# Kernel tuning notes

Hardware: AMD Instinct MI355X
Metric: run time of the kernel (lower is better)

## Reference

```python
import jax, jax.numpy as jnp
import numpy as np

N_NODES = 50000
N_EDGES = 800000
EMB = 128
HID = [128, 128]
OUT = 64
CE = 8  # stand-in for CROSS_ENTROPY_INDEXES: first 8 output columns get sigmoid


def _linear_params(key, d_in, d_out):
    k1, k2 = jax.random.split(key)
    s = 1.0 / np.sqrt(d_in)
    w = jax.random.uniform(k1, (d_in, d_out), minval=-s, maxval=s, dtype=jnp.float32)
    b = jax.random.uniform(k2, (d_out,), minval=-s, maxval=s, dtype=jnp.float32)
    return w, b


def setup_inputs() -> dict:
    key = jax.random.key(0)
    ks = jax.random.split(key, 16)
    z = jax.random.normal(ks[0], (N_NODES, EMB), dtype=jnp.float32)
    edge_index = jax.random.randint(ks[1], (2, N_EDGES), 0, N_NODES, dtype=jnp.int64)
    # SAGEConv params: neighbor weight (with bias) + root weight
    w1_n, b1 = _linear_params(ks[2], EMB, HID[0])
    w1_r, _ = _linear_params(ks[3], EMB, HID[0])
    w2_n, b2 = _linear_params(ks[4], HID[0], HID[1])
    w2_r, _ = _linear_params(ks[5], HID[0], HID[1])
    wf_n, bf = _linear_params(ks[6], HID[1], OUT)
    wf_r, _ = _linear_params(ks[7], HID[1], OUT)
    # initial residual linears: emb -> hid[1], emb -> out
    w_res1, b_res1 = _linear_params(ks[8], EMB, HID[1])
    w_res2, b_res2 = _linear_params(ks[9], EMB, OUT)
    return dict(z=z, edge_index=edge_index,
                w1_n=w1_n, w1_r=w1_r, b1=b1,
                w2_n=w2_n, w2_r=w2_r, b2=b2,
                wf_n=wf_n, wf_r=wf_r, bf=bf,
                w_res1=w_res1, b_res1=b_res1,
                w_res2=w_res2, b_res2=b_res2)


def _sage(x, src, dst, w_n, w_r, b, n_nodes):
    # mean-aggregate neighbor features at target nodes, then affine combine with root
    msg = x[src]                                        # [E, d]
    agg = jax.ops.segment_sum(msg, dst, num_segments=n_nodes)
    deg = jax.ops.segment_sum(jnp.ones_like(dst, dtype=x.dtype), dst, num_segments=n_nodes)
    mean = agg / jnp.maximum(deg, 1.0)[:, None]
    return mean @ w_n + x @ w_r + b


def reference(z, edge_index, w1_n, w1_r, b1, w2_n, w2_r, b2, wf_n, wf_r, bf,
              w_res1, b_res1, w_res2, b_res2):
    n = z.shape[0]
    src, dst = edge_index[0], edge_index[1]
    h = jax.nn.relu(_sage(z, src, dst, w1_n, w1_r, b1, n))
    # mid layer (dropout is identity in eval) + initial residual
    h = jax.nn.relu(_sage(h, src, dst, w2_n, w2_r, b2, n))
    h = h + (z @ w_res1 + b_res1)
    # final conv + final residual
    h = _sage(h, src, dst, wf_n, wf_r, bf, n)
    h = h + (z @ w_res2 + b_res2)
    # sigmoid on cross-entropy columns
    h = h.at[:, :CE].set(jax.nn.sigmoid(h[:, :CE]))
    return h
```

## Files before the change

kernel.cpp:

```cpp
#include <hip/hip_runtime.h>
#include <hip/hip_bf16.h>
#include <math.h>

#define NN 50000
#define NE 800000
#define NB 391
#define EPB 6250

typedef short bf16x8 __attribute__((ext_vector_type(8)));
typedef float f32x4 __attribute__((ext_vector_type(4)));
typedef unsigned short us4 __attribute__((ext_vector_type(4)));
typedef unsigned short us8 __attribute__((ext_vector_type(8)));
typedef unsigned int u32x4 __attribute__((ext_vector_type(4)));

__device__ __forceinline__ float bf2f(unsigned short u) {
  union { unsigned int i; float f; } x; x.i = ((unsigned int)u) << 16; return x.f;
}
__device__ __forceinline__ unsigned short f2bf(float f) {
  union { float f; unsigned int i; } x; x.f = f;
  unsigned int i = x.i;
  unsigned int r = i + 0x7FFF + ((i >> 16) & 1);
  return (unsigned short)(r >> 16);
}
__device__ __forceinline__ unsigned long long pk64(f32x4 v) {
  union { us4 s; unsigned long long u; } x;
  x.s[0] = f2bf(v[0]); x.s[1] = f2bf(v[1]); x.s[2] = f2bf(v[2]); x.s[3] = f2bf(v[3]);
  return x.u;
}
__device__ __forceinline__ us4 pack4(f32x4 v) {
  us4 o; o[0] = f2bf(v[0]); o[1] = f2bf(v[1]); o[2] = f2bf(v[2]); o[3] = f2bf(v[3]);
  return o;
}

__global__ __launch_bounds__(512) void bscan_kernel(const int* __restrict__ bhist,
                                                    int* __restrict__ bucket_off,
                                                    int* __restrict__ gcur) {
  __shared__ int s[512];
  int t = threadIdx.x;
  int v = (t < NB) ? bhist[t] : 0;
  s[t] = v; __syncthreads();
  for (int off = 1; off < 512; off <<= 1) {
    int x = (t >= off) ? s[t - off] : 0;
    __syncthreads();
    s[t] += x;
    __syncthreads();
  }
  if (t < NB) { bucket_off[t] = s[t] - v; gcur[t] = 0; }
  if (t == NB - 1) bucket_off[NB] = s[t];
}

__global__ __launch_bounds__(256) void bscat_kernel(const int* __restrict__ srcn,
                                                    const int* __restrict__ dstn,
                                                    const int* __restrict__ bucket_off,
                                                    int* __restrict__ gcur,
                                                    unsigned long long* __restrict__ ebuf) {
  __shared__ int hist[NB];
  __shared__ int base[NB];
  for (int i = threadIdx.x; i < NB; i += 256) hist[i] = 0;
  __syncthreads();
  int e0 = blockIdx.x * EPB;
  for (int i = threadIdx.x; i < EPB; i += 256)
    atomicAdd(&hist[dstn[e0 + i] >> 7], 1);
  __syncthreads();
  for (int i = threadIdx.x; i < NB; i += 256) {
    int c = hist[i];
    base[i] = c ? (bucket_off[i] + atomicAdd(&gcur[i], c)) : 0;
  }
  __syncthreads();
  for (int i = threadIdx.x; i < EPB; i += 256) {
    int s = srcn[e0 + i], d = dstn[e0 + i];
    int b = d >> 7;
    int pos = atomicSub(&hist[b], 1) - 1;
    ebuf[(size_t)base[b] + pos] = ((unsigned long long)(unsigned)d << 32) | (unsigned)s;
  }
}

__global__ __launch_bounds__(256) void bfill_kernel(const unsigned long long* __restrict__ ebuf,
                                                    const int* __restrict__ bucket_off,
                                                    int* __restrict__ rowoff,
                                                    int* __restrict__ csr) {
  int b = blockIdx.x;
  int bo = bucket_off[b], cnt = bucket_off[b + 1] - bo;
  __shared__ int ndeg[128], noff[128];
  int t = threadIdx.x;
  if (t < 128) ndeg[t] = 0;
  __syncthreads();
  for (int i = t; i < cnt; i += 256)
    atomicAdd(&ndeg[(int)(ebuf[bo + i] >> 32) & 127], 1);
  __syncthreads();
  if (t < 128) noff[t] = ndeg[t];
  __syncthreads();
  for (int off = 1; off < 128; off <<= 1) {
    int x = 0;
    if (t < 128 && t >= off) x = noff[t - off];
    __syncthreads();
    if (t < 128 && t >= off) noff[t] += x;
    __syncthreads();
  }
  if (t < 128) {
    int ex = noff[t] - ndeg[t];
    noff[t] = ex;
    int node = b * 128 + t;
    if (node < NN) rowoff[node] = bo + ex;
  }
  if (b == NB - 1 && t == 0) rowoff[NN] = NE;
  __syncthreads();
  for (int i = t; i < cnt; i += 256) {
    unsigned long long e = ebuf[bo + i];
    int dl = (int)(e >> 32) & 127;
    int pos = atomicSub(&ndeg[dl], 1) - 1;
    csr[bo + noff[dl] + pos] = (int)(unsigned)e;
  }
}

__global__ __launch_bounds__(256) void setup_kernel(
    const float* __restrict__ z, unsigned short* __restrict__ A1,
    const float* __restrict__ w1n, const float* __restrict__ w1r,
    const float* __restrict__ w2n, const float* __restrict__ w2r,
    const float* __restrict__ wfn, const float* __restrict__ wfr,
    const float* __restrict__ wr1, const float* __restrict__ wr2,
    unsigned short* __restrict__ Bp1, unsigned short* __restrict__ Bp2,
    unsigned short* __restrict__ Bp3,
    const int* __restrict__ dstn, int* __restrict__ bhist) {
  __shared__ int h[NB];
  int b = blockIdx.x;
  if (b < 6250) {
    int i = b * 256 + threadIdx.x;
    if (i >= NN * 128 / 4) return;
    int i4 = i * 4;
    int row = i4 >> 7, c = i4 & 127;
    f32x4 v = *(const f32x4*)(z + i4);
    us4 o = { f2bf(v[0]), f2bf(v[1]), f2bf(v[2]), f2bf(v[3]) };
    *(us4*)(A1 + (size_t)row * 256 + 128 + c) = o;
  } else if (b < 6314) {
    int g = (b - 6250) * 256 + threadIdx.x;
    unsigned short* D; int NT, fi;
    int which;
    if      (g < 10240) { fi = g;         D = Bp1; NT = 20; which = 1; }
    else if (g < 14336) { fi = g - 10240; D = Bp2; NT = 8;  which = 2; }
    else if (g < 16384) { fi = g - 14336; D = Bp3; NT = 4;  which = 3; }
    else return;
    int lane = fi & 63, t = fi >> 6;
    int nt = t % NT, k0i = t / NT;
    int m = lane & 15, q = lane >> 4;
    int kb = k0i * 32 + q * 8;
    int n = nt * 16 + m;
    int hi = (kb >= 128);
    int k0_ = kb - (hi ? 128 : 0);
    const float* W = nullptr; int Nseg = 128; int nn = n;
    if (which == 1) {
      if (n < 128)      { W = hi ? w1r : w1n; nn = n; Nseg = 128; }
      else if (n < 256) { W = hi ? wr1 : nullptr; nn = n - 128; Nseg = 128; }
      else              { W = hi ? wr2 : nullptr; nn = n - 256; Nseg = 64; }
    } else if (which == 2) { W = hi ? w2r : w2n; Nseg = 128; }
    else                   { W = hi ? wfr : wfn; Nseg = 64; }
    unsigned short o[8];
#pragma unroll
    for (int j = 0; j < 8; j++)
      o[j] = W ? f2bf(W[(size_t)(k0_ + j) * Nseg + nn]) : (unsigned short)0;
    *(us8*)(D + (size_t)fi * 8) = *(const us8*)o;
  } else {
    for (int i = threadIdx.x; i < NB; i += 256) h[i] = 0;
    __syncthreads();
    int e0 = (b - 6314) * EPB;
    for (int i = threadIdx.x; i < EPB; i += 256)
      atomicAdd(&h[dstn[e0 + i] >> 7], 1);
    __syncthreads();
    for (int i = threadIdx.x; i < NB; i += 256)
      if (h[i]) atomicAdd(&bhist[i], h[i]);
  }
}

__global__ __launch_bounds__(256) void agg_kernel(const unsigned short* __restrict__ feat, int fstride,
                                                  unsigned short* __restrict__ outm, int ostride,
                                                  const int* __restrict__ rowoff,
                                                  const int* __restrict__ csr) {
  int wave = threadIdx.x >> 6, lane = threadIdx.x & 63;
  int node = blockIdx.x * 4 + wave;
  if (node >= NN) return;
  int beg = rowoff[node], end = rowoff[node + 1];
  int g = lane >> 4;
  int c = (lane & 15) << 3;
  float a[8];
#pragma unroll
  for (int i = 0; i < 8; i++) a[i] = 0.f;
  int e1 = end - 1;
  for (int j = beg + g; j < end; j += 16) {
    int j1 = (j + 4 < e1) ? j + 4 : e1;
    int j2 = (j + 8 < e1) ? j + 8 : e1;
    int j3 = (j + 12 < e1) ? j + 12 : e1;
    int s0 = csr[j], s1 = csr[j1], s2 = csr[j2], s3 = csr[j3];
    float w1 = (j + 4 < end) ? 1.f : 0.f;
    float w2 = (j + 8 < end) ? 1.f : 0.f;
    float w3 = (j + 12 < end) ? 1.f : 0.f;
    u32x4 v0 = *(const u32x4*)(feat + (size_t)s0 * fstride + c);
    u32x4 v1 = *(const u32x4*)(feat + (size_t)s1 * fstride + c);
    u32x4 v2 = *(const u32x4*)(feat + (size_t)s2 * fstride + c);
    u32x4 v3 = *(const u32x4*)(feat + (size_t)s3 * fstride + c);
#pragma unroll
    for (int i = 0; i < 4; i++) {
      float l0 = bf2f((unsigned short)(v0[i] & 0xffff));
      float h0 = bf2f((unsigned short)(v0[i] >> 16));
      l0 = fmaf(w1, bf2f((unsigned short)(v1[i] & 0xffff)), l0);
      h0 = fmaf(w1, bf2f((unsigned short)(v1[i] >> 16)), h0);
      l0 = fmaf(w2, bf2f((unsigned short)(v2[i] & 0xffff)), l0);
      h0 = fmaf(w2, bf2f((unsigned short)(v2[i] >> 16)), h0);
      l0 = fmaf(w3, bf2f((unsigned short)(v3[i] & 0xffff)), l0);
      h0 = fmaf(w3, bf2f((unsigned short)(v3[i] >> 16)), h0);
      a[2*i] += l0;
      a[2*i+1] += h0;
    }
  }
#pragma unroll
  for (int i = 0; i < 8; i++) {
    a[i] += __shfl_xor(a[i], 16, 64);
    a[i] += __shfl_xor(a[i], 32, 64);
  }
  if (g == 0) {
    float inv = 1.f / fmaxf((float)(end - beg), 1.f);
    unsigned int o[4];
#pragma unroll
    for (int i = 0; i < 4; i++)
      o[i] = ((unsigned int)f2bf(a[2*i+1] * inv) << 16) | f2bf(a[2*i] * inv);
    *(u32x4*)(outm + (size_t)node * ostride + c) = *(const u32x4*)o;
  }
}

__global__ __launch_bounds__(256) void gemm1_kernel(
    const unsigned short* __restrict__ A,
    const unsigned short* __restrict__ Bp,
    const float* __restrict__ b1, const float* __restrict__ br1, const float* __restrict__ br2,
    unsigned short* __restrict__ h1out,
    unsigned short* __restrict__ res1, unsigned short* __restrict__ res2)
{
  const int NT = 20, TILES = 4;
  __shared__ unsigned short Bs[TILES * 8 * 512];
  int tid = threadIdx.x;
  int wave = tid >> 6, lane = tid & 63;
  int xg = blockIdx.x;
  int ybase = xg * TILES;
  int row0 = blockIdx.y * 128 + wave * 16;
  int m = lane & 15, q = lane >> 4;
  const float* bias; unsigned short* dst; int dstride, cbb; int relu;
  if (xg < 2)      { bias = b1 + xg * 64;        dst = h1out; dstride = 256; cbb = xg * 64;        relu = 1; }
  else if (xg < 4) { bias = br1 + (xg - 2) * 64; dst = res1;  dstride = 128; cbb = (xg - 2) * 64;  relu = 0; }
  else             { bias = br2;                 dst = res2;  dstride = 64;  cbb = 0;              relu = 0; }

  const unsigned short* arow0 = A + (size_t)(row0 + m) * 256 + q * 8;
  const unsigned short* arow1 = arow0 + 64 * 256;
  bf16x8 af0[8], af1[8];
#pragma unroll
  for (int k0i = 0; k0i < 8; ++k0i) {
    af0[k0i] = *(const bf16x8*)(arow0 + k0i * 32);
    af1[k0i] = *(const bf16x8*)(arow1 + k0i * 32);
  }
#pragma unroll
  for (int i = tid; i < TILES * 64 * 8; i += 256) {
    int k0i = i / (TILES * 64), r = i % (TILES * 64);
    *(us8*)(Bs + (size_t)k0i * TILES * 512 + (size_t)r * 8) =
        *(const us8*)(Bp + ((size_t)k0i * NT + ybase) * 512 + (size_t)r * 8);
  }
  __syncthreads();
  f32x4 acc[2][TILES];
#pragma unroll
  for (int h = 0; h < 2; h++)
#pragma unroll
    for (int i = 0; i < TILES; i++) acc[h][i] = (f32x4){0.f, 0.f, 0.f, 0.f};
#pragma unroll
  for (int k0i = 0; k0i < 8; ++k0i) {
    const unsigned short* bk = Bs + (size_t)k0i * TILES * 512 + lane * 8;
#pragma unroll
    for (int s = 0; s < TILES; ++s) {
      bf16x8 bfr = *(const bf16x8*)(bk + s * 512);
      acc[0][s] = __builtin_amdgcn_mfma_f32_16x16x32_bf16(bfr, af0[k0i], acc[0][s], 0, 0, 0);
      acc[1][s] = __builtin_amdgcn_mfma_f32_16x16x32_bf16(bfr, af1[k0i], acc[1][s], 0, 0, 0);
    }
  }
  int src0 = m + ((q & 1) ? 32 : 0);
#pragma unroll
  for (int h = 0; h < 2; h++) {
    int row = row0 + h * 64 + m;
#pragma unroll
    for (int p = 0; p < 2; p++) {
      f32x4 v0 = acc[h][2 * p], v1 = acc[h][2 * p + 1];
      f32x4 bb0 = *(const f32x4*)(bias + 32 * p + 4 * q);
      f32x4 bb1 = *(const f32x4*)(bias + 32 * p + 16 + 4 * q);
#pragma unroll
      for (int r = 0; r < 4; r++) { v0[r] += bb0[r]; v1[r] += bb1[r]; }
      if (relu) {
#pragma unroll
        for (int r = 0; r < 4; r++) { v0[r] = fmaxf(v0[r], 0.f); v1[r] = fmaxf(v1[r], 0.f); }
      }
      unsigned long long d0 = pk64(v0), d1 = pk64(v1);
      unsigned long long a0 = __shfl(d0, src0, 64);
      unsigned long long b0 = __shfl(d0, src0 + 16, 64);
      unsigned long long a1 = __shfl(d1, src0, 64);
      unsigned long long b1v = __shfl(d1, src0 + 16, 64);
      unsigned long long lo = (q >> 1) ? a1 : a0;
      unsigned long long hi = (q >> 1) ? b1v : b0;
      if (row < NN) {
        unsigned long long ov[2] = { lo, hi };
        *(us8*)(dst + (size_t)row * dstride + cbb + 32 * p + 8 * q) = *(const us8*)ov;
      }
    }
  }
}

__global__ __launch_bounds__(256) void gemm2_kernel(
    const unsigned short* __restrict__ A,
    const unsigned short* __restrict__ Bp,
    const float* __restrict__ b2,
    const unsigned short* __restrict__ res1,
    unsigned short* __restrict__ out_bf)
{
  const int NT = 8, TILES = 4;
  __shared__ unsigned short Bs[TILES * 8 * 512];
  int tid = threadIdx.x;
  int wave = tid >> 6, lane = tid & 63;
  int xg = blockIdx.x;
  int ybase = xg * TILES;
  int cbb = xg * 64;
  const float* bias = b2 + cbb;
  int row0 = blockIdx.y * 128 + wave * 16;
  int m = lane & 15, q = lane >> 4;
  const unsigned short* arow0 = A + (size_t)(row0 + m) * 256 + q * 8;
  const unsigned short* arow1 = arow0 + 64 * 256;
  bf16x8 af0[8], af1[8];
#pragma unroll
  for (int k0i = 0; k0i < 8; ++k0i) {
    af0[k0i] = *(const bf16x8*)(arow0 + k0i * 32);
    af1[k0i] = *(const bf16x8*)(arow1 + k0i * 32);
  }
#pragma unroll
  for (int i = tid; i < TILES * 64 * 8; i += 256) {
    int k0i = i / (TILES * 64), r = i % (TILES * 64);
    *(us8*)(Bs + (size_t)k0i * TILES * 512 + (size_t)r * 8) =
        *(const us8*)(Bp + ((size_t)k0i * NT + ybase) * 512 + (size_t)r * 8);
  }
  __syncthreads();
  f32x4 acc[2][TILES];
#pragma unroll
  for (int h = 0; h < 2; h++)
#pragma unroll
    for (int i = 0; i < TILES; i++) acc[h][i] = (f32x4){0.f, 0.f, 0.f, 0.f};
#pragma unroll
  for (int k0i = 0; k0i < 8; ++k0i) {
    const unsigned short* bk = Bs + (size_t)k0i * TILES * 512 + lane * 8;
#pragma unroll
    for (int s = 0; s < TILES; ++s) {
      bf16x8 bfr = *(const bf16x8*)(bk + s * 512);
      acc[0][s] = __builtin_amdgcn_mfma_f32_16x16x32_bf16(bfr, af0[k0i], acc[0][s], 0, 0, 0);
      acc[1][s] = __builtin_amdgcn_mfma_f32_16x16x32_bf16(bfr, af1[k0i], acc[1][s], 0, 0, 0);
    }
  }
  int src0 = m + ((q & 1) ? 32 : 0);
#pragma unroll
  for (int h = 0; h < 2; h++) {
    int row = row0 + h * 64 + m;
#pragma unroll
    for (int p = 0; p < 2; p++) {
      f32x4 v0 = acc[h][2 * p], v1 = acc[h][2 * p + 1];
      f32x4 bb0 = *(const f32x4*)(bias + 32 * p + 4 * q);
      f32x4 bb1 = *(const f32x4*)(bias + 32 * p + 16 + 4 * q);
#pragma unroll
      for (int r = 0; r < 4; r++) {
        v0[r] = fmaxf(v0[r] + bb0[r], 0.f);
        v1[r] = fmaxf(v1[r] + bb1[r], 0.f);
      }
      unsigned long long d0 = pk64(v0), d1 = pk64(v1);
      unsigned long long a0 = __shfl(d0, src0, 64);
      unsigned long long b0 = __shfl(d0, src0 + 16, 64);
      unsigned long long a1 = __shfl(d1, src0, 64);
      unsigned long long b1v = __shfl(d1, src0 + 16, 64);
      unsigned long long lo = (q >> 1) ? a1 : a0;
      unsigned long long hi = (q >> 1) ? b1v : b0;
      if (row < NN) {
        size_t off = cbb + 32 * p + 8 * q;
        us8 rv = *(const us8*)(res1 + (size_t)row * 128 + off);
        unsigned long long ov[2] = { lo, hi };
        unsigned short* e = (unsigned short*)ov;
#pragma unroll
        for (int r = 0; r < 8; r++) e[r] = f2bf(bf2f(e[r]) + bf2f(rv[r]));
        *(us8*)(out_bf + (size_t)row * 256 + off) = *(const us8*)ov;
      }
    }
  }
}

__global__ __launch_bounds__(256) void gemm3_kernel(
    const unsigned short* __restrict__ A,
    const unsigned short* __restrict__ Bp,
    const float* __restrict__ bias,
    const unsigned short* __restrict__ res2,
    float* __restrict__ out_f)
{
  const int NT = 4, TILES = 4;
  __shared__ unsigned short Bs[TILES * 8 * 512];
  int tid = threadIdx.x;
  int wave = tid >> 6, lane = tid & 63;
  int row0 = blockIdx.y * 64 + wave * 16;
  int m = lane & 15, q = lane >> 4;
  const unsigned short* arow = A + (size_t)(row0 + m) * 256 + q * 8;
  bf16x8 af[8];
#pragma unroll
  for (int k0i = 0; k0i < 8; ++k0i) af[k0i] = *(const bf16x8*)(arow + k0i * 32);
#pragma unroll
  for (int i = tid; i < TILES * 64 * 8; i += 256) {
    int k0i = i / (TILES * 64), r = i % (TILES * 64);
    *(us8*)(Bs + (size_t)k0i * TILES * 512 + (size_t)r * 8) =
        *(const us8*)(Bp + ((size_t)k0i * NT) * 512 + (size_t)r * 8);
  }
  __syncthreads();
  f32x4 acc[TILES];
#pragma unroll
  for (int i = 0; i < TILES; i++) acc[i] = (f32x4){0.f, 0.f, 0.f, 0.f};
#pragma unroll
  for (int k0i = 0; k0i < 8; ++k0i) {
    const unsigned short* bk = Bs + (size_t)k0i * TILES * 512 + lane * 8;
#pragma unroll
    for (int s = 0; s < TILES; ++s) {
      bf16x8 bfr = *(const bf16x8*)(bk + s * 512);
      acc[s] = __builtin_amdgcn_mfma_f32_16x16x32_bf16(bfr, af[k0i], acc[s], 0, 0, 0);
    }
  }
  int row = row0 + m;
  if (row >= NN) return;
  int cb = q * 4;
#pragma unroll
  for (int s = 0; s < TILES; ++s) {
    int col = s * 16 + cb;
    f32x4 v = acc[s];
    f32x4 bb = *(const f32x4*)(bias + col);
    us4 rv = *(const us4*)(res2 + (size_t)row * 64 + col);
#pragma unroll
    for (int r = 0; r < 4; r++) v[r] += bb[r] + bf2f(rv[r]);
    if (col < 8) {
#pragma unroll
      for (int r = 0; r < 4; r++) v[r] = 1.f / (1.f + __expf(-v[r]));
    }
    *(f32x4*)(out_f + (size_t)row * 64 + col) = v;
  }
}

extern "C" void kernel_launch(void* const* d_in, const int* in_sizes, int n_in,
                              void* d_out, int out_size, void* d_ws, size_t ws_size,
                              hipStream_t stream) {
  const float* z   = (const float*)d_in[0];
  const int*   edge = (const int*)d_in[1];
  const int*   srcn = edge;
  const int*   dstn = edge + NE;
  const float* w1n = (const float*)d_in[2];
  const float* w1r = (const float*)d_in[3];
  const float* b1  = (const float*)d_in[4];
  const float* w2n = (const float*)d_in[5];
  const float* w2r = (const float*)d_in[6];
  const float* b2  = (const float*)d_in[7];
  const float* wfn = (const float*)d_in[8];
  const float* wfr = (const float*)d_in[9];
  const float* bfb = (const float*)d_in[10];
  const float* wr1 = (const float*)d_in[11];
  const float* br1 = (const float*)d_in[12];
  const float* wr2 = (const float*)d_in[13];
  const float* br2 = (const float*)d_in[14];
  float* out = (float*)d_out;

  char* p = (char*)d_ws;
  auto alloc = [&](size_t bytes) { char* r = p; p += (bytes + 255) & ~255ull; return r; };
  int* rowoff = (int*)alloc((size_t)(NN + 1) * 4);
  int* bhist  = (int*)alloc((size_t)NB * 4);
  int* bucket_off = (int*)alloc((size_t)(NB + 1) * 4);
  int* gcur   = (int*)alloc((size_t)NB * 4);
  int* csr    = (int*)alloc((size_t)NE * 4);
  unsigned short* A1 = (unsigned short*)alloc((size_t)NN * 256 * 2);
  unsigned short* A2 = (unsigned short*)alloc((size_t)NN * 256 * 2);
  unsigned short* res1 = (unsigned short*)alloc((size_t)NN * 128 * 2);
  unsigned short* res2 = (unsigned short*)alloc((size_t)NN * 64 * 2);
  unsigned short* Bp1 = (unsigned short*)alloc(10240 * 8 * 2);
  unsigned short* Bp2 = (unsigned short*)alloc(4096 * 8 * 2);
  unsigned short* Bp3 = (unsigned short*)alloc(2048 * 8 * 2);
  unsigned short* A3 = A1;
  unsigned long long* ebuf = (unsigned long long*)res1;

  hipMemsetAsync(bhist, 0, (size_t)NB * 4, stream);
  setup_kernel<<<6442, 256, 0, stream>>>(z, A1, w1n, w1r, w2n, w2r, wfn, wfr, wr1, wr2,
                                         Bp1, Bp2, Bp3, dstn, bhist);
  bscan_kernel<<<1, 512, 0, stream>>>(bhist, bucket_off, gcur);
  bscat_kernel<<<128, 256, 0, stream>>>(srcn, dstn, bucket_off, gcur, ebuf);
  bfill_kernel<<<NB, 256, 0, stream>>>(ebuf, bucket_off, rowoff, csr);

  const int gy128 = (NN + 127) / 128;
  const int gy64  = (NN + 63) / 64;
  const int agg_blocks = (NN + 3) / 4;

  agg_kernel<<<agg_blocks, 256, 0, stream>>>(A1 + 128, 256, A1, 256, rowoff, csr);
  gemm1_kernel<<<dim3(5, gy128), 256, 0, stream>>>(A1, Bp1, b1, br1, br2, A2 + 128, res1, res2);

  agg_kernel<<<agg_blocks, 256, 0, stream>>>(A2 + 128, 256, A2, 256, rowoff, csr);
  gemm2_kernel<<<dim3(2, gy128), 256, 0, stream>>>(A2, Bp2, b2, res1, A3 + 128);

  agg_kernel<<<agg_blocks, 256, 0, stream>>>(A3 + 128, 256, A3, 256, rowoff, csr);
  gemm3_kernel<<<dim3(1, gy64), 256, 0, stream>>>(A3, Bp3, bfb, res2, out);
}
```

Measured before the change: 282.3 us.

## Move residual GEMMs into the first aggregation launch to overlap with gather

The two initial-residual projections (z@w_res1 and z@w_res2) move out of gemm1 and into a combined aggregation launch. Blocks past the aggregation range run those GEMM tiles, so MFMA work shares the GPU with the memory-bound neighbour gather, and gemm1 shrinks to the two ReLU tiles. The edge scratch buffer moves from res1 to A2 because res1 is now written during the first aggregation. One risk: the residual tiles read the full 256-column rows of A1 while other blocks are still writing its mean half. This relies on the packed weights being zero there and on those values being finite.

```diff
diff --git a/kernel.cpp b/kernel.cpp
--- a/kernel.cpp
+++ b/kernel.cpp
@@ -26,10 +26,6 @@
   union { us4 s; unsigned long long u; } x;
   x.s[0] = f2bf(v[0]); x.s[1] = f2bf(v[1]); x.s[2] = f2bf(v[2]); x.s[3] = f2bf(v[3]);
   return x.u;
-}
-__device__ __forceinline__ us4 pack4(f32x4 v) {
-  us4 o; o[0] = f2bf(v[0]); o[1] = f2bf(v[1]); o[2] = f2bf(v[2]); o[3] = f2bf(v[3]);
-  return o;
 }
 
 __global__ __launch_bounds__(512) void bscan_kernel(const int* __restrict__ bhist,
@@ -171,12 +167,11 @@
   }
 }
 
-__global__ __launch_bounds__(256) void agg_kernel(const unsigned short* __restrict__ feat, int fstride,
-                                                  unsigned short* __restrict__ outm, int ostride,
-                                                  const int* __restrict__ rowoff,
-                                                  const int* __restrict__ csr) {
-  int wave = threadIdx.x >> 6, lane = threadIdx.x & 63;
-  int node = blockIdx.x * 4 + wave;
+__device__ __forceinline__ void agg_node(const unsigned short* __restrict__ feat, int fstride,
+                                         unsigned short* __restrict__ outm, int ostride,
+                                         const int* __restrict__ rowoff,
+                                         const int* __restrict__ csr,
+                                         int node, int lane) {
   if (node >= NN) return;
   int beg = rowoff[node], end = rowoff[node + 1];
   int g = lane >> 4;
@@ -226,12 +221,100 @@
   }
 }
 
+__global__ __launch_bounds__(256) void agg_kernel(const unsigned short* __restrict__ feat, int fstride,
+                                                  unsigned short* __restrict__ outm, int ostride,
+                                                  const int* __restrict__ rowoff,
+                                                  const int* __restrict__ csr) {
+  agg_node(feat, fstride, outm, ostride, rowoff, csr,
+           blockIdx.x * 4 + (threadIdx.x >> 6), threadIdx.x & 63);
+}
+
+__global__ __launch_bounds__(256) void aggres_kernel(
+    const unsigned short* __restrict__ A,
+    unsigned short* __restrict__ outm,
+    const int* __restrict__ rowoff, const int* __restrict__ csr,
+    const unsigned short* __restrict__ Bp,
+    const float* __restrict__ br1, const float* __restrict__ br2,
+    unsigned short* __restrict__ res1, unsigned short* __restrict__ res2)
+{
+  const int NT = 20, TILES = 4;
+  __shared__ unsigned short Bs[TILES * 8 * 512];
+  int b = blockIdx.x;
+  if (b < 12500) {
+    agg_node(A + 128, 256, outm, 256, rowoff, csr,
+             b * 4 + (threadIdx.x >> 6), threadIdx.x & 63);
+    return;
+  }
+  int g = b - 12500;
+  int xg, y; const float* bias; unsigned short* dst; int dstride, cbb, ybase;
+  if (g < 782) { xg = g & 1; y = g >> 1; ybase = 8 + xg * 4; bias = br1 + xg * 64;
+                 dst = res1; dstride = 128; cbb = xg * 64; }
+  else { g -= 782; xg = 0; y = g; ybase = 16; bias = br2; dst = res2; dstride = 64; cbb = 0; }
+  int tid = threadIdx.x;
+  int wave = tid >> 6, lane = tid & 63;
+  int row0 = y * 128 + wave * 16;
+  int m = lane & 15, q = lane >> 4;
+  const unsigned short* arow0 = A + (size_t)(row0 + m) * 256 + q * 8;
+  const unsigned short* arow1 = arow0 + 64 * 256;
+  bf16x8 af0[8], af1[8];
+#pragma unroll
+  for (int k0i = 0; k0i < 8; ++k0i) {
+    af0[k0i] = *(const bf16x8*)(arow0 + k0i * 32);
+    af1[k0i] = *(const bf16x8*)(arow1 + k0i * 32);
+  }
+#pragma unroll
+  for (int i = tid; i < TILES * 64 * 8; i += 256) {
+    int k0i = i / (TILES * 64), r = i % (TILES * 64);
+    *(us8*)(Bs + (size_t)k0i * TILES * 512 + (size_t)r * 8) =
+        *(const us8*)(Bp + ((size_t)k0i * NT + ybase) * 512 + (size_t)r * 8);
+  }
+  __syncthreads();
+  f32x4 acc[2][TILES];
+#pragma unroll
+  for (int h = 0; h < 2; h++)
+#pragma unroll
+    for (int i = 0; i < TILES; i++) acc[h][i] = (f32x4){0.f, 0.f, 0.f, 0.f};
+#pragma unroll
+  for (int k0i = 0; k0i < 8; ++k0i) {
+    const unsigned short* bk = Bs + (size_t)k0i * TILES * 512 + lane * 8;
+#pragma unroll
+    for (int s = 0; s < TILES; ++s) {
+      bf16x8 bfr = *(const bf16x8*)(bk + s * 512);
+      acc[0][s] = __builtin_amdgcn_mfma_f32_16x16x32_bf16(bfr, af0[k0i], acc[0][s], 0, 0, 0);
+      acc[1][s] = __builtin_amdgcn_mfma_f32_16x16x32_bf16(bfr, af1[k0i], acc[1][s], 0, 0, 0);
+    }
+  }
+  int src0 = m + ((q & 1) ? 32 : 0);
+#pragma unroll
+  for (int h = 0; h < 2; h++) {
+    int row = row0 + h * 64 + m;
+#pragma unroll
+    for (int p = 0; p < 2; p++) {
+      f32x4 v0 = acc[h][2 * p], v1 = acc[h][2 * p + 1];
+      f32x4 bb0 = *(const f32x4*)(bias + 32 * p + 4 * q);
+      f32x4 bb1 = *(const f32x4*)(bias + 32 * p + 16 + 4 * q);
+#pragma unroll
+      for (int r = 0; r < 4; r++) { v0[r] += bb0[r]; v1[r] += bb1[r]; }
+      unsigned long long d0 = pk64(v0), d1 = pk64(v1);
+      unsigned long long a0 = __shfl(d0, src0, 64);
+      unsigned long long b0 = __shfl(d0, src0 + 16, 64);
+      unsigned long long a1 = __shfl(d1, src0, 64);
+      unsigned long long b1v = __shfl(d1, src0 + 16, 64);
+      unsigned long long lo = (q >> 1) ? a1 : a0;
+      unsigned long long hi = (q >> 1) ? b1v : b0;
+      if (row < NN) {
+        unsigned long long ov[2] = { lo, hi };
+        *(us8*)(dst + (size_t)row * dstride + cbb + 32 * p + 8 * q) = *(const us8*)ov;
+      }
+    }
+  }
+}
+
 __global__ __launch_bounds__(256) void gemm1_kernel(
     const unsigned short* __restrict__ A,
     const unsigned short* __restrict__ Bp,
-    const float* __restrict__ b1, const float* __restrict__ br1, const float* __restrict__ br2,
-    unsigned short* __restrict__ h1out,
-    unsigned short* __restrict__ res1, unsigned short* __restrict__ res2)
+    const float* __restrict__ b1,
+    unsigned short* __restrict__ h1out)
 {
   const int NT = 20, TILES = 4;
   __shared__ unsigned short Bs[TILES * 8 * 512];
@@ -239,13 +322,10 @@
   int wave = tid >> 6, lane = tid & 63;
   int xg = blockIdx.x;
   int ybase = xg * TILES;
+  int cbb = xg * 64;
+  const float* bias = b1 + cbb;
   int row0 = blockIdx.y * 128 + wave * 16;
   int m = lane & 15, q = lane >> 4;
-  const float* bias; unsigned short* dst; int dstride, cbb; int relu;
-  if (xg < 2)      { bias = b1 + xg * 64;        dst = h1out; dstride = 256; cbb = xg * 64;        relu = 1; }
-  else if (xg < 4) { bias = br1 + (xg - 2) * 64; dst = res1;  dstride = 128; cbb = (xg - 2) * 64;  relu = 0; }
-  else             { bias = br2;                 dst = res2;  dstride = 64;  cbb = 0;              relu = 0; }
-
   const unsigned short* arow0 = A + (size_t)(row0 + m) * 256 + q * 8;
   const unsigned short* arow1 = arow0 + 64 * 256;
   bf16x8 af0[8], af1[8];
@@ -286,10 +366,9 @@
       f32x4 bb0 = *(const f32x4*)(bias + 32 * p + 4 * q);
       f32x4 bb1 = *(const f32x4*)(bias + 32 * p + 16 + 4 * q);
 #pragma unroll
-      for (int r = 0; r < 4; r++) { v0[r] += bb0[r]; v1[r] += bb1[r]; }
-      if (relu) {
-#pragma unroll
-        for (int r = 0; r < 4; r++) { v0[r] = fmaxf(v0[r], 0.f); v1[r] = fmaxf(v1[r], 0.f); }
+      for (int r = 0; r < 4; r++) {
+        v0[r] = fmaxf(v0[r] + bb0[r], 0.f);
+        v1[r] = fmaxf(v1[r] + bb1[r], 0.f);
       }
       unsigned long long d0 = pk64(v0), d1 = pk64(v1);
       unsigned long long a0 = __shfl(d0, src0, 64);
@@ -300,7 +379,7 @@
       unsigned long long hi = (q >> 1) ? b1v : b0;
       if (row < NN) {
         unsigned long long ov[2] = { lo, hi };
-        *(us8*)(dst + (size_t)row * dstride + cbb + 32 * p + 8 * q) = *(const us8*)ov;
+        *(us8*)(h1out + (size_t)row * 256 + cbb + 32 * p + 8 * q) = *(const us8*)ov;
       }
     }
   }
@@ -479,7 +558,7 @@
   unsigned short* Bp2 = (unsigned short*)alloc(4096 * 8 * 2);
   unsigned short* Bp3 = (unsigned short*)alloc(2048 * 8 * 2);
   unsigned short* A3 = A1;
-  unsigned long long* ebuf = (unsigned long long*)res1;
+  unsigned long long* ebuf = (unsigned long long*)A2;
 
   hipMemsetAsync(bhist, 0, (size_t)NB * 4, stream);
   setup_kernel<<<6442, 256, 0, stream>>>(z, A1, w1n, w1r, w2n, w2r, wfn, wfr, wr1, wr2,
@@ -492,8 +571,9 @@
   const int gy64  = (NN + 63) / 64;
   const int agg_blocks = (NN + 3) / 4;
 
-  agg_kernel<<<agg_blocks, 256, 0, stream>>>(A1 + 128, 256, A1, 256, rowoff, csr);
-  gemm1_kernel<<<dim3(5, gy128), 256, 0, stream>>>(A1, Bp1, b1, br1, br2, A2 + 128, res1, res2);
+  aggres_kernel<<<agg_blocks + 3 * gy128, 256, 0, stream>>>(
+      A1, A1, rowoff, csr, Bp1, br1, br2, res1, res2);
+  gemm1_kernel<<<dim3(2, gy128), 256, 0, stream>>>(A1, Bp1, b1, A2 + 128);
 
   agg_kernel<<<agg_blocks, 256, 0, stream>>>(A2 + 128, 256, A2, 256, rowoff, csr);
   gemm2_kernel<<<dim3(2, gy128), 256, 0, stream>>>(A2, Bp2, b2, res1, A3 + 128);
```

Result: slower. 297.6 us (+5.4%).
